# Optimization experiments

Hardware: AMD Instinct MI355X
Metric: run time of the kernel (lower is better)

The kernel has to match this reference:

```python
import jax, jax.numpy as jnp
import numpy as np

H = 32      # n_heads
KV = 8      # n_kv_heads
HD = 64     # head_dim = dim // n_heads


def setup_inputs() -> dict:
    key = jax.random.key(0)
    ks = jax.random.split(key, 8)
    B, S, D = 4, 1024, 2048
    x = jax.random.normal(ks[0], (B, S, D), dtype=jnp.float32)
    # RoPE tables stored as cos/sin parts of the complex freqs_cis (seqlen, head_dim//2)
    pos = jnp.arange(S, dtype=jnp.float32)[:, None]
    inv = 1.0 / (10000.0 ** (jnp.arange(0, HD, 2, dtype=jnp.float32) / HD))[None, :]
    ang = pos * inv                          # (S, HD//2)
    freqs_cos = jnp.cos(ang)
    freqs_sin = jnp.sin(ang)
    # additive causal mask (S, S): 0 on/below diagonal, -inf above
    mask = jnp.where(jnp.tril(jnp.ones((S, S), dtype=bool)), 0.0, -jnp.inf).astype(jnp.float32)
    sc = 0.02
    wq = jax.random.normal(ks[1], (H * HD, D), dtype=jnp.float32) * sc
    wk = jax.random.normal(ks[2], (KV * HD, D), dtype=jnp.float32) * sc
    wv = jax.random.normal(ks[3], (KV * HD, D), dtype=jnp.float32) * sc
    wo = jax.random.normal(ks[4], (D, D), dtype=jnp.float32) * sc
    return {"x": x, "freqs_cos": freqs_cos, "freqs_sin": freqs_sin, "mask": mask,
            "wq": wq, "wk": wk, "wv": wv, "wo": wo}


def _rope(t, cos, sin):
    # t: (B, S, nh, HD). Faithful to source: rotation is indexed by x.shape[2]
    # (the HEAD axis, due to pre-transpose call), broadcast over sequence.
    nh = t.shape[2]
    c = cos[:nh][None, None, :, :]           # (1,1,nh,HD//2)
    s = sin[:nh][None, None, :, :]
    tr = t.reshape(*t.shape[:-1], HD // 2, 2)
    t0, t1 = tr[..., 0], tr[..., 1]
    o0 = t0 * c - t1 * s
    o1 = t0 * s + t1 * c
    return jnp.stack([o0, o1], axis=-1).reshape(t.shape)


def reference(x, freqs_cos, freqs_sin, mask, wq, wk, wv, wo):
    B, S, D = x.shape
    xq = (x @ wq.T).reshape(B, S, H, HD)
    xk = (x @ wk.T).reshape(B, S, KV, HD)
    xv = (x @ wv.T).reshape(B, S, KV, HD)
    xq = _rope(xq, freqs_cos, freqs_sin)
    xk = _rope(xk, freqs_cos, freqs_sin)
    rep = H // KV
    xk = jnp.repeat(xk, rep, axis=2)         # GQA repeat_interleave on head axis
    xv = jnp.repeat(xv, rep, axis=2)
    q = xq.transpose(0, 2, 1, 3)             # (B,H,S,HD)
    k = xk.transpose(0, 2, 1, 3)
    v = xv.transpose(0, 2, 1, 3)
    scores = jnp.einsum('bhqd,bhkd->bhqk', q, k) / np.sqrt(HD).astype(np.float32)
    scores = scores + mask[None, None, :, :]
    p = jax.nn.softmax(scores.astype(jnp.float32), axis=-1).astype(q.dtype)
    out = jnp.einsum('bhqk,bhkd->bhqd', p, v)
    out = out.transpose(0, 2, 1, 3).reshape(B, S, H * HD)
    return out @ wo.T
```

## Files before the change

kernel.cpp:

```cpp
#include <hip/hip_runtime.h>
#include <hip/hip_bf16.h>

constexpr int kB  = 4;
constexpr int kS  = 1024;
constexpr int kD  = 2048;
constexpr int kH  = 32;
constexpr int kKV = 8;
constexpr int kHD = 64;
constexpr int kM  = kB * kS;
constexpr int kNT = kS / 64;

constexpr float kNegBig = -30000.0f;
constexpr float kC = 0.125f * 1.44269504f;
constexpr float kDeferThr = 40.0f;

typedef __attribute__((ext_vector_type(8))) short short8;
typedef __attribute__((ext_vector_type(4))) float floatx4;

static __device__ __forceinline__ float bf2f(short v) {
    unsigned int u = ((unsigned int)(unsigned short)v) << 16;
    return __builtin_bit_cast(float, u);
}
static __device__ __forceinline__ short f2bf(float f) {
    unsigned int u = __builtin_bit_cast(unsigned int, f);
    unsigned int lsb = (u >> 16) & 1u;
    u += 0x7fffu + lsb;
    return (short)(u >> 16);
}
static __device__ __forceinline__ short f2bf_fast(float f) {
    unsigned int u = __builtin_bit_cast(unsigned int, f);
    return (short)((u + 0x8000u) >> 16);
}

static __device__ __forceinline__ void load_lds16(const short* g, short* l) {
    __builtin_amdgcn_global_load_lds(
        (const __attribute__((address_space(1))) unsigned int*)g,
        (__attribute__((address_space(3))) unsigned int*)l, 16, 0, 0);
}

__global__ void cast_f2b(const float* __restrict__ in, short* __restrict__ outp, int n4) {
    int gid = blockIdx.x * blockDim.x + threadIdx.x;
    if (gid >= n4) return;
    float4 v = ((const float4*)in)[gid];
    short4 o;
    o.x = f2bf(v.x); o.y = f2bf(v.y); o.z = f2bf(v.z); o.w = f2bf(v.w);
    ((short4*)outp)[gid] = o;
}

template <typename OT, int ROPE>
__global__ __launch_bounds__(256) void gemm_bt_lds(const short* __restrict__ A,
                                                   const short* __restrict__ Bm,
                                                   OT* __restrict__ C,
                                                   int M, int N, int K,
                                                   const float* __restrict__ cosb,
                                                   const float* __restrict__ sinb,
                                                   short* __restrict__ Vt) {
    __shared__ short As[128 * 32];
    __shared__ short Bs[128 * 32];

    int tid  = threadIdx.x;
    int wave = tid >> 6, lane = tid & 63;
    int quad = lane >> 4, l16 = lane & 15;
    int wm = wave >> 1, wn = wave & 1;

    int nwg  = gridDim.x * gridDim.y;
    int orig = blockIdx.y * gridDim.x + blockIdx.x;
    int wg   = orig;
    if ((nwg & 7) == 0) {
        int cpx = nwg >> 3;
        wg = (orig & 7) * cpx + (orig >> 3);
    }
    int bx = wg % gridDim.x, by = wg / gridDim.x;
    int m0 = by * 128, n0 = bx * 128;

    floatx4 acc[4][4];
    for (int i = 0; i < 4; i++)
        for (int j = 0; j < 4; j++) acc[i][j] = (floatx4){0.f, 0.f, 0.f, 0.f};

    int srow = lane >> 2;
    int skc  = (lane & 3) * 8;

    for (int k0 = 0; k0 < K; k0 += 32) {
        __syncthreads();
        for (int i = 0; i < 2; i++) {
            int r16 = wave * 32 + i * 16;
            load_lds16(A + (long)(m0 + r16 + srow) * K + k0 + skc, &As[r16 * 32]);
            load_lds16(Bm + (long)(n0 + r16 + srow) * K + k0 + skc, &Bs[r16 * 32]);
        }
        __syncthreads();

        short8 af[4], bfr[4];
        for (int i = 0; i < 4; i++)
            af[i] = *(const short8*)&As[(wm * 64 + i * 16 + l16) * 32 + quad * 8];
        for (int j = 0; j < 4; j++)
            bfr[j] = *(const short8*)&Bs[(wn * 64 + j * 16 + l16) * 32 + quad * 8];
        for (int i = 0; i < 4; i++)
            for (int j = 0; j < 4; j++)
                acc[i][j] = __builtin_amdgcn_mfma_f32_16x16x32_bf16(
                    af[i], bfr[j], acc[i][j], 0, 0, 0);
    }

    for (int j = 0; j < 4; j++) {
        int col = n0 + wn * 64 + j * 16 + l16;

        if constexpr (ROPE == 2) {
            if (col >= 512) {
                int cv = col - 512;
                for (int i = 0; i < 4; i++) {
                    int row0 = m0 + wm * 64 + i * 16 + quad * 4;
                    short4 o;
                    o.x = f2bf(acc[i][j][0]);
                    o.y = f2bf(acc[i][j][1]);
                    o.z = f2bf(acc[i][j][2]);
                    o.w = f2bf(acc[i][j][3]);
                    *(short4*)&Vt[(long)cv * M + row0] = o;
                }
                continue;
            }
        }

        float c = 0.f, s = 0.f;
        bool rope_col = (ROPE == 1) || (ROPE == 2 && col < 512);
        if constexpr (ROPE != 0) {
            if (rope_col) {
                int hh = col >> 6;
                int ii = (col & 63) >> 1;
                c = cosb[hh * 32 + ii];
                s = sinb[hh * 32 + ii];
            }
        }
        for (int i = 0; i < 4; i++) {
            for (int r = 0; r < 4; r++) {
                int row = m0 + wm * 64 + i * 16 + quad * 4 + r;
                float v = acc[i][j][r];
                if constexpr (ROPE != 0) {
                    float p = __shfl_xor(v, 1);
                    if (rope_col)
                        v = (col & 1) ? (p * s + v * c)
                                      : (v * c - p * s);
                }
                if constexpr (sizeof(OT) == 2)
                    C[(long)row * N + col] = f2bf(v);
                else
                    C[(long)row * N + col] = v;
            }
        }
    }
}

__global__ __launch_bounds__(256) void attn_kernel(const short* __restrict__ xq,
                                                   const short* __restrict__ xk,
                                                   const short* __restrict__ vt,
                                                   short* __restrict__ out,
                                                   int kvstride) {
    __shared__ short pT[4][16][72];

    int pb = blockIdx.x;
    int h = blockIdx.y, b = blockIdx.z;
    int kvh = h >> 2;
    int tid = threadIdx.x, wave = tid >> 6, lane = tid & 63;
    int quad = lane >> 4, l16 = lane & 15;

    const short* kbase0 = xk + (long)b * kS * kvstride + kvh * kHD;
    const short* vbase = vt + (long)kvh * kHD * kM + (long)b * kS;

    short8 ones;
    for (int i = 0; i < 8; i++) ones[i] = (short)0x3F80;

    auto loadK = [&](short8 (&kf)[4][2], int kt) {
        const short* kbase = kbase0 + (long)kt * 64 * kvstride;
        for (int kb = 0; kb < 4; kb++) {
            const short* kp = kbase + (long)(kb * 16 + l16) * kvstride + quad * 8;
            kf[kb][0] = *(const short8*)kp;
            kf[kb][1] = *(const short8*)(kp + 32);
        }
    };

    for (int qi = 0; qi < 2; qi++) {
        int qb = (qi == 0) ? (kNT - 1 - pb) : pb;
        int nt = qb + 1;
        int wr0  = qb * 64 + wave * 16;
        int qrow = wr0 + l16;
        int crow = wr0 + quad * 4;

        const short* qp = xq + (((long)b * kS + qrow) * kH + h) * kHD + quad * 8;
        short8 qf0 = *(const short8*)(qp);
        short8 qf1 = *(const short8*)(qp + 32);

        float m_run[4];
        floatx4 acc_l = (floatx4){0.f, 0.f, 0.f, 0.f};
        floatx4 acc_o[4];
        for (int r = 0; r < 4; r++) m_run[r] = kNegBig;
        for (int nb = 0; nb < 4; nb++) acc_o[nb] = (floatx4){0.f, 0.f, 0.f, 0.f};

        auto step = [&](short8 (&kf)[4][2], int kt) {
            floatx4 accs[4];
            __builtin_amdgcn_s_setprio(1);
            for (int kb = 0; kb < 4; kb++) {
                accs[kb] = (floatx4){0.f, 0.f, 0.f, 0.f};
                accs[kb] = __builtin_amdgcn_mfma_f32_16x16x32_bf16(qf0, kf[kb][0], accs[kb], 0, 0, 0);
                accs[kb] = __builtin_amdgcn_mfma_f32_16x16x32_bf16(qf1, kf[kb][1], accs[kb], 0, 0, 0);
            }
            __builtin_amdgcn_s_setprio(0);

            short8 vf[4][2];
            for (int nb = 0; nb < 4; nb++) {
                const short* vp = vbase + (long)(nb * 16 + l16) * kM + kt * 64 + quad * 8;
                vf[nb][0] = *(const short8*)(vp);
                vf[nb][1] = *(const short8*)(vp + 32);
            }

            if (kt == nt - 1) {
                for (int kb = 0; kb < 4; kb++)
                    for (int r = 0; r < 4; r++) {
                        int kj = kt * 64 + kb * 16 + l16;
                        if (kj > crow + r) accs[kb][r] = kNegBig;
                    }
            }

            float mx[4];
            for (int r = 0; r < 4; r++) {
                float m1 = fmaxf(fmaxf(accs[0][r], accs[1][r]),
                                 fmaxf(accs[2][r], accs[3][r]));
                for (int off = 1; off < 16; off <<= 1) m1 = fmaxf(m1, __shfl_xor(m1, off));
                mx[r] = m1;
            }
            bool small = (mx[0] - m_run[0] <= kDeferThr) && (mx[1] - m_run[1] <= kDeferThr) &&
                         (mx[2] - m_run[2] <= kDeferThr) && (mx[3] - m_run[3] <= kDeferThr);
            if (!__all(small)) {
                for (int r = 0; r < 4; r++) {
                    float mnew = fmaxf(m_run[r], mx[r]);
                    float alpha = exp2f((m_run[r] - mnew) * kC);
                    m_run[r] = mnew;
                    acc_l[r] *= alpha;
                    for (int nb = 0; nb < 4; nb++) acc_o[nb][r] *= alpha;
                }
            }

            for (int r = 0; r < 4; r++) {
                float mk = m_run[r] * kC;
                for (int kb = 0; kb < 4; kb++)
                    accs[kb][r] = exp2f(fmaf(accs[kb][r], kC, -mk));
            }

            for (int r = 0; r < 4; r++)
                for (int kb = 0; kb < 4; kb++)
                    pT[wave][quad * 4 + r][kb * 16 + l16] = f2bf_fast(accs[kb][r]);

            short8 pf0 = *(const short8*)&pT[wave][l16][quad * 8];
            short8 pf1 = *(const short8*)&pT[wave][l16][32 + quad * 8];
            __builtin_amdgcn_s_setprio(1);
            acc_l = __builtin_amdgcn_mfma_f32_16x16x32_bf16(pf0, ones, acc_l, 0, 0, 0);
            acc_l = __builtin_amdgcn_mfma_f32_16x16x32_bf16(pf1, ones, acc_l, 0, 0, 0);
            for (int nb = 0; nb < 4; nb++) {
                acc_o[nb] = __builtin_amdgcn_mfma_f32_16x16x32_bf16(pf0, vf[nb][0], acc_o[nb], 0, 0, 0);
                acc_o[nb] = __builtin_amdgcn_mfma_f32_16x16x32_bf16(pf1, vf[nb][1], acc_o[nb], 0, 0, 0);
            }
            __builtin_amdgcn_s_setprio(0);
        };

        short8 kfA[4][2], kfB[4][2];
        loadK(kfA, 0);
        int kt = 0;
        while (true) {
            if (kt + 1 < nt) loadK(kfB, kt + 1);
            step(kfA, kt);
            if (++kt >= nt) break;
            if (kt + 1 < nt) loadK(kfA, kt + 1);
            step(kfB, kt);
            if (++kt >= nt) break;
        }

        for (int r = 0; r < 4; r++) {
            float inv = 1.0f / fmaxf(acc_l[r], 1e-20f);
            int row = crow + r;
            for (int nb = 0; nb < 4; nb++)
                out[(((long)b * kS + row) * kH + h) * kHD + nb * 16 + l16] =
                    f2bf(acc_o[nb][r] * inv);
        }
    }
}

extern "C" void kernel_launch(void* const* d_in, const int* in_sizes, int n_in,
                              void* d_out, int out_size, void* d_ws, size_t ws_size,
                              hipStream_t stream) {
    const float* x  = (const float*)d_in[0];
    const float* fc = (const float*)d_in[1];
    const float* fs = (const float*)d_in[2];
    const float* wq = (const float*)d_in[4];
    const float* wk = (const float*)d_in[5];
    const float* wv = (const float*)d_in[6];
    const float* wo = (const float*)d_in[7];

    const int M = kM;
    const long MB = 1l << 20;

    char* ws = (char*)d_ws;
    short* xb   = (short*)(ws);
    short* wqb  = (short*)(ws + 16 * MB);
    short* wkvb = (short*)(ws + 16 * MB);
    short* ao   = (short*)(ws);
    short* wob  = (short*)(ws + 16 * MB);
    char*  dob  = (char*)d_out;
    short* xq   = (short*)(dob);
    short* xkv  = (short*)(dob + 16 * MB);
    short* vt   = (short*)(dob + 24 * MB);

    const int nX  = M * kD;
    const int nWq = kD * kD;
    const int nWk = kKV * kHD * kD;

    cast_f2b<<<(nX / 4 + 255) / 256, 256, 0, stream>>>(x, xb, nX / 4);
    cast_f2b<<<(nWq / 4 + 255) / 256, 256, 0, stream>>>(wq, wqb, nWq / 4);
    gemm_bt_lds<short, 1><<<dim3(kD / 128, M / 128), 256, 0, stream>>>(
        xb, wqb, xq, M, kD, kD, fc, fs, nullptr);

    cast_f2b<<<(nWk / 4 + 255) / 256, 256, 0, stream>>>(wk, wkvb, nWk / 4);
    cast_f2b<<<(nWk / 4 + 255) / 256, 256, 0, stream>>>(wv, wkvb + nWk, nWk / 4);
    gemm_bt_lds<short, 2><<<dim3(1024 / 128, M / 128), 256, 0, stream>>>(
        xb, wkvb, xkv, M, 1024, kD, fc, fs, vt);

    attn_kernel<<<dim3(kS / 128, kH, kB), 256, 0, stream>>>(
        xq, xkv, vt, ao, 1024);

    cast_f2b<<<(nWq / 4 + 255) / 256, 256, 0, stream>>>(wo, wob, nWq / 4);
    gemm_bt_lds<float, 0><<<dim3(kD / 128, M / 128), 256, 0, stream>>>(
        ao, wob, (float*)d_out, M, kD, kD, nullptr, nullptr, nullptr);
}
```

Baseline: 412.2 us.

## Fuse Q/K/V projections into one GEMM and batch input casts

Merges the four fp32-to-bf16 cast launches for x, wq, wk and wv into a single kernel. It also fuses the Q projection and the K/V projection into one 3072-wide GEMM whose epilogue routes columns to Q (with RoPE), K (with RoPE) or transposed V. The K/V weight staging buffer moves into the output buffer so it does not overlap wq. In attention, the double-buffered K prefetch with lambda steps becomes a single-buffered loop with V loaded earlier, and occupancy is hinted to 4 blocks per SIMD via launch bounds. Together these aim to cut launch count and give the projection GEMM a larger grid, at the risk of register pressure or exposed K latency in attention.

```diff
diff --git a/kernel.cpp b/kernel.cpp
--- a/kernel.cpp
+++ b/kernel.cpp
@@ -17,10 +17,6 @@
 typedef __attribute__((ext_vector_type(8))) short short8;
 typedef __attribute__((ext_vector_type(4))) float floatx4;
 
-static __device__ __forceinline__ float bf2f(short v) {
-    unsigned int u = ((unsigned int)(unsigned short)v) << 16;
-    return __builtin_bit_cast(float, u);
-}
 static __device__ __forceinline__ short f2bf(float f) {
     unsigned int u = __builtin_bit_cast(unsigned int, f);
     unsigned int lsb = (u >> 16) & 1u;
@@ -47,6 +43,24 @@
     ((short4*)outp)[gid] = o;
 }
 
+__global__ void cast4_f2b(const float* __restrict__ a, const float* __restrict__ b,
+                          const float* __restrict__ c, const float* __restrict__ d,
+                          short* __restrict__ oa, short* __restrict__ ob,
+                          short* __restrict__ oc, short* __restrict__ od,
+                          int na4, int nb4, int nc4, int nd4) {
+    int gid = blockIdx.x * blockDim.x + threadIdx.x;
+    const float* src; short* dst; int idx;
+    if (gid < na4)                    { src = a; dst = oa; idx = gid; }
+    else if (gid < na4 + nb4)         { src = b; dst = ob; idx = gid - na4; }
+    else if (gid < na4 + nb4 + nc4)   { src = c; dst = oc; idx = gid - na4 - nb4; }
+    else if (gid < na4+nb4+nc4+nd4)   { src = d; dst = od; idx = gid - na4 - nb4 - nc4; }
+    else return;
+    float4 v = ((const float4*)src)[idx];
+    short4 o;
+    o.x = f2bf(v.x); o.y = f2bf(v.y); o.z = f2bf(v.z); o.w = f2bf(v.w);
+    ((short4*)dst)[idx] = o;
+}
+
 template <typename OT, int ROPE>
 __global__ __launch_bounds__(256) void gemm_bt_lds(const short* __restrict__ A,
                                                    const short* __restrict__ Bm,
@@ -54,7 +68,9 @@
                                                    int M, int N, int K,
                                                    const float* __restrict__ cosb,
                                                    const float* __restrict__ sinb,
-                                                   short* __restrict__ Vt) {
+                                                   short* __restrict__ Vt,
+                                                   const short* __restrict__ B2,
+                                                   short* __restrict__ Kout) {
     __shared__ short As[128 * 32];
     __shared__ short Bs[128 * 32];
 
@@ -73,6 +89,12 @@
     int bx = wg % gridDim.x, by = wg / gridDim.x;
     int m0 = by * 128, n0 = bx * 128;
 
+    const short* Bblk;
+    if constexpr (ROPE == 3)
+        Bblk = (n0 < 2048) ? Bm + (long)n0 * K : B2 + (long)(n0 - 2048) * K;
+    else
+        Bblk = Bm + (long)n0 * K;
+
     floatx4 acc[4][4];
     for (int i = 0; i < 4; i++)
         for (int j = 0; j < 4; j++) acc[i][j] = (floatx4){0.f, 0.f, 0.f, 0.f};
@@ -85,7 +107,7 @@
         for (int i = 0; i < 2; i++) {
             int r16 = wave * 32 + i * 16;
             load_lds16(A + (long)(m0 + r16 + srow) * K + k0 + skc, &As[r16 * 32]);
-            load_lds16(Bm + (long)(n0 + r16 + srow) * K + k0 + skc, &Bs[r16 * 32]);
+            load_lds16(Bblk + (long)(r16 + srow) * K + k0 + skc, &Bs[r16 * 32]);
         }
         __syncthreads();
 
@@ -100,12 +122,11 @@
                     af[i], bfr[j], acc[i][j], 0, 0, 0);
     }
 
-    for (int j = 0; j < 4; j++) {
-        int col = n0 + wn * 64 + j * 16 + l16;
-
-        if constexpr (ROPE == 2) {
-            if (col >= 512) {
-                int cv = col - 512;
+    if constexpr (ROPE == 3) {
+        for (int j = 0; j < 4; j++) {
+            int col = n0 + wn * 64 + j * 16 + l16;
+            if (col >= 2560) {
+                int cv = col - 2560;
                 for (int i = 0; i < 4; i++) {
                     int row0 = m0 + wm * 64 + i * 16 + quad * 4;
                     short4 o;
@@ -115,44 +136,48 @@
                     o.w = f2bf(acc[i][j][3]);
                     *(short4*)&Vt[(long)cv * M + row0] = o;
                 }
-                continue;
-            }
-        }
-
-        float c = 0.f, s = 0.f;
-        bool rope_col = (ROPE == 1) || (ROPE == 2 && col < 512);
-        if constexpr (ROPE != 0) {
-            if (rope_col) {
-                int hh = col >> 6;
+            } else {
+                bool isK = col >= 2048;
+                int hh = isK ? ((col - 2048) >> 6) : (col >> 6);
                 int ii = (col & 63) >> 1;
-                c = cosb[hh * 32 + ii];
-                s = sinb[hh * 32 + ii];
-            }
-        }
-        for (int i = 0; i < 4; i++) {
-            for (int r = 0; r < 4; r++) {
-                int row = m0 + wm * 64 + i * 16 + quad * 4 + r;
-                float v = acc[i][j][r];
-                if constexpr (ROPE != 0) {
-                    float p = __shfl_xor(v, 1);
-                    if (rope_col)
+                float c = cosb[hh * 32 + ii];
+                float s = sinb[hh * 32 + ii];
+                for (int i = 0; i < 4; i++) {
+                    for (int r = 0; r < 4; r++) {
+                        int row = m0 + wm * 64 + i * 16 + quad * 4 + r;
+                        float v = acc[i][j][r];
+                        float p = __shfl_xor(v, 1);
                         v = (col & 1) ? (p * s + v * c)
                                       : (v * c - p * s);
+                        if (isK)
+                            Kout[(long)row * 1024 + (col - 2048)] = f2bf(v);
+                        else
+                            ((short*)C)[(long)row * 2048 + col] = f2bf(v);
+                    }
                 }
-                if constexpr (sizeof(OT) == 2)
-                    C[(long)row * N + col] = f2bf(v);
-                else
-                    C[(long)row * N + col] = v;
-            }
+            }
+        }
+    } else {
+        for (int j = 0; j < 4; j++) {
+            int col = n0 + wn * 64 + j * 16 + l16;
+            for (int i = 0; i < 4; i++)
+                for (int r = 0; r < 4; r++) {
+                    int row = m0 + wm * 64 + i * 16 + quad * 4 + r;
+                    float v = acc[i][j][r];
+                    if constexpr (sizeof(OT) == 2)
+                        C[(long)row * N + col] = f2bf(v);
+                    else
+                        C[(long)row * N + col] = v;
+                }
         }
     }
 }
 
-__global__ __launch_bounds__(256) void attn_kernel(const short* __restrict__ xq,
-                                                   const short* __restrict__ xk,
-                                                   const short* __restrict__ vt,
-                                                   short* __restrict__ out,
-                                                   int kvstride) {
+__global__ __launch_bounds__(256, 4) void attn_kernel(const short* __restrict__ xq,
+                                                      const short* __restrict__ xk,
+                                                      const short* __restrict__ vt,
+                                                      short* __restrict__ out,
+                                                      int kvstride) {
     __shared__ short pT[4][16][72];
 
     int pb = blockIdx.x;
@@ -193,7 +218,17 @@
         for (int r = 0; r < 4; r++) m_run[r] = kNegBig;
         for (int nb = 0; nb < 4; nb++) acc_o[nb] = (floatx4){0.f, 0.f, 0.f, 0.f};
 
-        auto step = [&](short8 (&kf)[4][2], int kt) {
+        short8 kf[4][2];
+        loadK(kf, 0);
+
+        for (int kt = 0; kt < nt; kt++) {
+            short8 vf[4][2];
+            for (int nb = 0; nb < 4; nb++) {
+                const short* vp = vbase + (long)(nb * 16 + l16) * kM + kt * 64 + quad * 8;
+                vf[nb][0] = *(const short8*)(vp);
+                vf[nb][1] = *(const short8*)(vp + 32);
+            }
+
             floatx4 accs[4];
             __builtin_amdgcn_s_setprio(1);
             for (int kb = 0; kb < 4; kb++) {
@@ -203,12 +238,7 @@
             }
             __builtin_amdgcn_s_setprio(0);
 
-            short8 vf[4][2];
-            for (int nb = 0; nb < 4; nb++) {
-                const short* vp = vbase + (long)(nb * 16 + l16) * kM + kt * 64 + quad * 8;
-                vf[nb][0] = *(const short8*)(vp);
-                vf[nb][1] = *(const short8*)(vp + 32);
-            }
+            if (kt + 1 < nt) loadK(kf, kt + 1);
 
             if (kt == nt - 1) {
                 for (int kb = 0; kb < 4; kb++)
@@ -257,18 +287,6 @@
                 acc_o[nb] = __builtin_amdgcn_mfma_f32_16x16x32_bf16(pf1, vf[nb][1], acc_o[nb], 0, 0, 0);
             }
             __builtin_amdgcn_s_setprio(0);
-        };
-
-        short8 kfA[4][2], kfB[4][2];
-        loadK(kfA, 0);
-        int kt = 0;
-        while (true) {
-            if (kt + 1 < nt) loadK(kfB, kt + 1);
-            step(kfA, kt);
-            if (++kt >= nt) break;
-            if (kt + 1 < nt) loadK(kfA, kt + 1);
-            step(kfB, kt);
-            if (++kt >= nt) break;
         }
 
         for (int r = 0; r < 4; r++) {
@@ -298,32 +316,30 @@
     char* ws = (char*)d_ws;
     short* xb   = (short*)(ws);
     short* wqb  = (short*)(ws + 16 * MB);
-    short* wkvb = (short*)(ws + 16 * MB);
     short* ao   = (short*)(ws);
     short* wob  = (short*)(ws + 16 * MB);
     char*  dob  = (char*)d_out;
     short* xq   = (short*)(dob);
     short* xkv  = (short*)(dob + 16 * MB);
     short* vt   = (short*)(dob + 24 * MB);
+    short* wkvb = (short*)(dob + 28 * MB);
 
     const int nX  = M * kD;
     const int nWq = kD * kD;
     const int nWk = kKV * kHD * kD;
 
-    cast_f2b<<<(nX / 4 + 255) / 256, 256, 0, stream>>>(x, xb, nX / 4);
-    cast_f2b<<<(nWq / 4 + 255) / 256, 256, 0, stream>>>(wq, wqb, nWq / 4);
-    gemm_bt_lds<short, 1><<<dim3(kD / 128, M / 128), 256, 0, stream>>>(
-        xb, wqb, xq, M, kD, kD, fc, fs, nullptr);
-
-    cast_f2b<<<(nWk / 4 + 255) / 256, 256, 0, stream>>>(wk, wkvb, nWk / 4);
-    cast_f2b<<<(nWk / 4 + 255) / 256, 256, 0, stream>>>(wv, wkvb + nWk, nWk / 4);
-    gemm_bt_lds<short, 2><<<dim3(1024 / 128, M / 128), 256, 0, stream>>>(
-        xb, wkvb, xkv, M, 1024, kD, fc, fs, vt);
+    int total4 = (nX + nWq + 2 * nWk) / 4;
+    cast4_f2b<<<(total4 + 255) / 256, 256, 0, stream>>>(
+        x, wq, wk, wv, xb, wqb, wkvb, wkvb + nWk,
+        nX / 4, nWq / 4, nWk / 4, nWk / 4);
+
+    gemm_bt_lds<short, 3><<<dim3(3072 / 128, M / 128), 256, 0, stream>>>(
+        xb, wqb, xq, M, 3072, kD, fc, fs, vt, wkvb, xkv);
 
     attn_kernel<<<dim3(kS / 128, kH, kB), 256, 0, stream>>>(
         xq, xkv, vt, ao, 1024);
 
     cast_f2b<<<(nWq / 4 + 255) / 256, 256, 0, stream>>>(wo, wob, nWq / 4);
     gemm_bt_lds<float, 0><<<dim3(kD / 128, M / 128), 256, 0, stream>>>(
-        ao, wob, (float*)d_out, M, kD, kD, nullptr, nullptr, nullptr);
-}
+        ao, wob, (float*)d_out, M, kD, kD, nullptr, nullptr, nullptr, nullptr, nullptr);
+}
```

After: 477.7 us. 15.9% more time.
